# Kernel tuning notes

Hardware: AMD Instinct MI355X
Metric: run time of the kernel (lower is better)

The kernel has to match this reference:

```python
import jax, jax.numpy as jnp
import numpy as np

HEAD_DIM = 128
N_HEADS = 32
NEG_INF = -1e9


def apply_rope(x, cos, sin):
    # x: (B, S, H, D); cos/sin: (S, D//2). Pairs (x[...,2i], x[...,2i+1]) form
    # complex numbers (torch.view_as_complex on reshape(..., -1, 2)).
    xr = x[..., 0::2]
    xi = x[..., 1::2]
    c = cos[None, :, None, :]
    s = sin[None, :, None, :]
    out_r = xr * c - xi * s
    out_i = xr * s + xi * c
    return jnp.stack([out_r, out_i], axis=-1).reshape(x.shape)


def setup_inputs() -> dict:
    key = jax.random.key(0)
    ks = jax.random.split(key, 8)
    B, S, D = 2, 1024, 4096
    hd = HEAD_DIM
    x = jax.random.normal(ks[0], (B, S, D), dtype=jnp.float32)
    # true RoPE frequencies
    theta = 10000.0 ** (-np.arange(0, hd, 2, dtype=np.float32) / hd)  # (hd/2,)
    angles = np.arange(S, dtype=np.float32)[:, None] * theta[None, :]  # (S, hd/2)
    freqs_cos = jnp.asarray(np.cos(angles))
    freqs_sin = jnp.asarray(np.sin(angles))
    # causal additive mask
    mask = jnp.where(jnp.triu(jnp.ones((S, S), dtype=bool), k=1), NEG_INF, 0.0)
    mask = mask[None, None, :, :].astype(jnp.float32)
    scale = 0.02
    wq = jax.random.normal(ks[1], (D, D), dtype=jnp.float32) * scale
    wk = jax.random.normal(ks[2], (D, D), dtype=jnp.float32) * scale
    wv = jax.random.normal(ks[3], (D, D), dtype=jnp.float32) * scale
    wo = jax.random.normal(ks[4], (D, D), dtype=jnp.float32) * scale
    cache_k = jnp.zeros((B, S, N_HEADS, hd), dtype=jnp.float32)
    cache_v = jnp.zeros((B, S, N_HEADS, hd), dtype=jnp.float32)
    return {
        "x": x, "start_pos": 0, "freqs_cos": freqs_cos, "freqs_sin": freqs_sin,
        "mask": mask, "cache_k": cache_k, "cache_v": cache_v,
        "wq": wq, "wk": wk, "wv": wv, "wo": wo,
    }


def reference(x, start_pos, freqs_cos, freqs_sin, mask, cache_k, cache_v, wq, wk, wv, wo):
    B, S, D = x.shape
    H, hd = N_HEADS, HEAD_DIM
    # QKV projections (torch Linear: y = x @ W.T)
    xq = jnp.einsum('bsd,od->bso', x, wq).reshape(B, S, H, hd)
    xk = jnp.einsum('bsd,od->bso', x, wk).reshape(B, S, H, hd)
    xv = jnp.einsum('bsd,od->bso', x, wv).reshape(B, S, H, hd)
    xq = apply_rope(xq, freqs_cos, freqs_sin)
    xk = apply_rope(xk, freqs_cos, freqs_sin)
    # KV-cache append (n_rep == 1, so repeat_kv is identity)
    cache_k = jax.lax.dynamic_update_slice(cache_k, xk, (0, start_pos, 0, 0))
    cache_v = jax.lax.dynamic_update_slice(cache_v, xv, (0, start_pos, 0, 0))
    kv_len = start_pos + S
    keys = cache_k[:, :kv_len]
    values = cache_v[:, :kv_len]
    # attention: energy -> mask -> scaled softmax -> weighted sum
    energy = jnp.einsum('bqhd,bkhd->bhqk', xq, keys)
    energy = energy + mask
    scores = jax.nn.softmax(energy.astype(jnp.float32) / jnp.sqrt(jnp.float32(hd)), axis=-1).astype(xq.dtype)
    out = jnp.einsum('bhqk,bkhd->bqhd', scores, values).reshape(B, S, H * hd)
    return jnp.einsum('bso,do->bsd', out, wo)
```

## Files before the change

### kernel.cpp

```cpp
#include <hip/hip_runtime.h>
#include <hip/hip_bf16.h>
#include <stdint.h>
#include <stddef.h>

typedef __bf16 bf16_t;
typedef __attribute__((ext_vector_type(8))) __bf16 bf16x8;
typedef __attribute__((ext_vector_type(4))) float f32x4;
typedef __attribute__((ext_vector_type(16))) float f32x16;
typedef __attribute__((ext_vector_type(4))) uint32_t u32x4;

#define D_MODEL 4096
#define SEQ 1024
#define NH 32
#define HD 128
#define MTOT 2048

#define VMCNT(n) asm volatile("s_waitcnt vmcnt(" #n ")" ::: "memory")
#define LGKM0() asm volatile("s_waitcnt lgkmcnt(0)" ::: "memory")
#define SCHED0() __builtin_amdgcn_sched_barrier(0)

__device__ __forceinline__ void gload_lds16(const void* g, void* l) {
  __builtin_amdgcn_global_load_lds((const __attribute__((address_space(1))) uint32_t*)g,
                                   (__attribute__((address_space(3))) uint32_t*)l, 16, 0, 0);
}

__device__ __forceinline__ uint32_t cvtpk(float lo, float hi) {
  uint32_t r;
  asm("v_cvt_pk_bf16_f32 %0, %1, %2" : "=v"(r) : "v"(lo), "v"(hi));
  return r;
}
__device__ __forceinline__ void plswap(uint32_t& a, uint32_t& b) {
  asm volatile("v_permlane32_swap_b32 %0, %1" : "+v"(a), "+v"(b));
}

__global__ void dtype_probe(const uint32_t* __restrict__ x, uint32_t* __restrict__ flag) {
  const int lane = threadIdx.x & 63;
  const uint32_t w = x[lane];
  const uint32_t e = (w >> 7) & 0xFF;
  const bool inband = (e >= 100 && e <= 140);
  const unsigned long long m = __ballot(inband);
  if (lane == 0) *flag = (__popcll(m) >= 32) ? 1u : 0u;
}

__global__ __launch_bounds__(256) void conv_bf16(const void* __restrict__ src,
                                                 bf16_t* __restrict__ dst, int n,
                                                 const uint32_t* __restrict__ flag) {
  const int i = (blockIdx.x * 256 + threadIdx.x) * 8;
  if (i >= n) return;
  if (*flag) {
    *(bf16x8*)(dst + i) = *(const bf16x8*)((const bf16_t*)src + i);
  } else {
    const float4 a = *(const float4*)((const float*)src + i);
    const float4 b = *(const float4*)((const float*)src + i + 4);
    bf16x8 v;
    v[0] = (bf16_t)a.x; v[1] = (bf16_t)a.y; v[2] = (bf16_t)a.z; v[3] = (bf16_t)a.w;
    v[4] = (bf16_t)b.x; v[5] = (bf16_t)b.y; v[6] = (bf16_t)b.z; v[7] = (bf16_t)b.w;
    *(bf16x8*)(dst + i) = v;
  }
}

template <int MODE>
__global__ __launch_bounds__(512, 2) void gemm_bt(
    const bf16_t* __restrict__ A, const bf16_t* __restrict__ B,
    void* __restrict__ dstv, const uint32_t* __restrict__ flagp,
    const bf16_t* __restrict__ fcos, const bf16_t* __restrict__ fsin) {
  __shared__ __align__(16) char smem[3 * 49152];
  const int tid = threadIdx.x;
  const int lane = tid & 63, wid = tid >> 6;
  const int fr = lane & 15, fq = lane >> 4;
  const int wm = wid >> 2, wn = wid & 3;
  const int bm0 = blockIdx.x * 128, bn0 = blockIdx.y * 256;
  const bool isbf = (MODE == 2) ? (*flagp != 0) : true;

  auto stage_half = [&](int t, int bi, int h) {
    const int k0 = t * 64;
    char* ab = smem + bi * 49152;
    char* bb = ab + 16384;
    {
      const int o = h * 8192 + tid * 16;
      const int row = o >> 7, ch = (o >> 4) & 7;
      gload_lds16(A + (size_t)(bm0 + row) * D_MODEL + k0 + ((ch ^ (row & 7)) * 8), ab + o);
    }
#pragma unroll
    for (int j = 0; j < 2; ++j) {
      const int o = (h * 2 + j) * 8192 + tid * 16;
      const int row = o >> 7, ch = (o >> 4) & 7;
      gload_lds16(B + (size_t)(bn0 + row) * D_MODEL + k0 + ((ch ^ (row & 7)) * 8), bb + o);
    }
  };

  f32x4 acc[4][4];
#pragma unroll
  for (int m = 0; m < 4; m++)
#pragma unroll
    for (int n = 0; n < 4; n++) acc[m][n] = f32x4{0.f, 0.f, 0.f, 0.f};

  auto phase = [&](int bi, int kk, bool do_stage, int ts, int bs, int h) {
    const char* ab = smem + bi * 49152;
    const char* bb = ab + 16384;
    const int swz = ((kk * 4 + fq) ^ (fr & 7)) << 4;
    bf16x8 af[4], bfv[4];
#pragma unroll
    for (int m = 0; m < 4; ++m)
      af[m] = *(const bf16x8*)(ab + (wm * 64 + m * 16 + fr) * 128 + swz);
#pragma unroll
    for (int n = 0; n < 4; ++n)
      bfv[n] = *(const bf16x8*)(bb + (wn * 64 + n * 16 + fr) * 128 + swz);
    if (do_stage) stage_half(ts, bs, h);
    __builtin_amdgcn_s_barrier();
    LGKM0();
    SCHED0();
    __builtin_amdgcn_s_setprio(1);
#pragma unroll
    for (int m = 0; m < 4; ++m)
#pragma unroll
      for (int n = 0; n < 4; ++n)
        acc[m][n] = __builtin_amdgcn_mfma_f32_16x16x32_bf16(af[m], bfv[n], acc[m][n], 0, 0, 0);
    __builtin_amdgcn_s_setprio(0);
  };

  const int NT = D_MODEL / 64;
  stage_half(0, 0, 0); stage_half(0, 0, 1);
  stage_half(1, 1, 0); stage_half(1, 1, 1);
  VMCNT(6);
  __builtin_amdgcn_s_barrier();
  SCHED0();
  int cur = 0, nxt = 2;
  for (int t = 0; t < NT - 2; ++t) {
    phase(cur, 0, true, t + 2, nxt, 0);
    __builtin_amdgcn_s_barrier();
    phase(cur, 1, true, t + 2, nxt, 1);
    VMCNT(6);
    __builtin_amdgcn_s_barrier();
    SCHED0();
    cur = (cur == 2) ? 0 : cur + 1;
    nxt = (nxt == 2) ? 0 : nxt + 1;
  }
  phase(cur, 0, false, 0, 0, 0);
  __builtin_amdgcn_s_barrier();
  phase(cur, 1, false, 0, 0, 0);
  VMCNT(0);
  __builtin_amdgcn_s_barrier();
  SCHED0();
  cur = (cur == 2) ? 0 : cur + 1;
  phase(cur, 0, false, 0, 0, 0);
  __builtin_amdgcn_s_barrier();
  phase(cur, 1, false, 0, 0, 0);

#pragma unroll
  for (int m = 0; m < 4; m++) {
#pragma unroll
    for (int n = 0; n < 4; n++) {
      const int gn = bn0 + wn * 64 + n * 16 + fr;
#pragma unroll
      for (int r = 0; r < 4; r++) {
        const int gm = bm0 + wm * 64 + m * 16 + fq * 4 + r;
        const float vv = acc[m][n][r];
        if constexpr (MODE == 0) {
          const float pv = __shfl_xor(vv, 1);
          const int s = gm & (SEQ - 1);
          const int i = (gn & (HD - 1)) >> 1;
          const float c = (float)fcos[s * 64 + i];
          const float si = (float)fsin[s * 64 + i];
          const float outv = (gn & 1) ? (pv * si + vv * c) : (vv * c - pv * si);
          const int b = gm >> 10, h = gn >> 7, dd = gn & (HD - 1);
          ((bf16_t*)dstv)[((size_t)(b * NH + h) * SEQ + s) * HD + dd] = (bf16_t)outv;
        } else if constexpr (MODE == 1) {
          const int b = gm >> 10, s = gm & (SEQ - 1), h = gn >> 7, dd = gn & (HD - 1);
          ((bf16_t*)dstv)[((size_t)(b * NH + h) * HD + dd) * SEQ + s] = (bf16_t)vv;
        } else {
          if (isbf) ((bf16_t*)dstv)[(size_t)gm * D_MODEL + gn] = (bf16_t)vv;
          else      ((float*)dstv)[(size_t)gm * D_MODEL + gn] = vv;
        }
      }
    }
  }
}

__global__ __launch_bounds__(512, 2) void attn_fwd(
    const bf16_t* __restrict__ Q, const bf16_t* __restrict__ K,
    const bf16_t* __restrict__ V, bf16_t* __restrict__ Out) {
  constexpr float SC = 0.088388347648318447f;
  constexpr float MNEG = -10000.0f;
  __shared__ __align__(16) char smem[65536];
  const int tid = threadIdx.x, lane = tid & 63, wid = tid >> 6;
  const int l31 = lane & 31, hi = lane >> 5, l7 = lane & 7;
  const int qt = 3 - (int)blockIdx.x;
  const int bh = blockIdx.y;
  const int qb0 = qt * 256;
  const int q0w = qb0 + wid * 32;
  const int nt = qt * 4 + 4;

  const bf16_t* Kbase = K + (size_t)bh * SEQ * HD;
  const bf16_t* Vbase = V + (size_t)bh * HD * SEQ;

  bf16x8 qa[8];
  {
    const bf16_t* qp = Q + ((size_t)bh * SEQ + q0w + l31) * HD + hi * 8;
#pragma unroll
    for (int ks = 0; ks < 8; ++ks) qa[ks] = *(const bf16x8*)(qp + ks * 16);
  }

  auto stage = [&](int t, int bi) {
    const int kv0 = t * 64;
#pragma unroll
    for (int pass = 0; pass < 2; ++pass) {
      const int o = pass * 8192 + tid * 16;
      {
        const int row = o >> 8, ch = (o & 255) >> 4;
        gload_lds16(Kbase + (size_t)(kv0 + row) * HD + ((ch ^ (row & 7)) * 8),
                    smem + bi * 16384 + o);
      }
      {
        const int row = o >> 7, ch = (o & 127) >> 4;
        gload_lds16(Vbase + (size_t)row * SEQ + kv0 + ((ch ^ (row & 7)) * 8),
                    smem + 32768 + bi * 16384 + o);
      }
    }
  };

  f32x16 Oacc[4];
#pragma unroll
  for (int i = 0; i < 4; ++i)
#pragma unroll
    for (int j = 0; j < 16; ++j) Oacc[i][j] = 0.f;
  float mrow = MNEG, lrow = 0.f;

  stage(0, 0);
  stage(1, 1);
  VMCNT(4);
  __builtin_amdgcn_s_barrier();

  for (int t = 0; t < nt; ++t) {
    const int kv0 = t * 64;
    if (kv0 < q0w + 32) {
      const char* kb_ = smem + (t & 1) * 16384;
      const char* vb_ = smem + 32768 + (t & 1) * 16384;

      f32x16 sacc[2];
#pragma unroll
      for (int kb = 0; kb < 2; ++kb)
#pragma unroll
        for (int j = 0; j < 16; ++j) sacc[kb][j] = 0.f;
      __builtin_amdgcn_s_setprio(1);
#pragma unroll
      for (int kb = 0; kb < 2; ++kb)
#pragma unroll
        for (int ks = 0; ks < 8; ++ks) {
          bf16x8 kf = *(const bf16x8*)(kb_ + (kb * 32 + l31) * 256 +
                                       (((ks * 2 + hi) ^ l7) << 4));
          sacc[kb] = __builtin_amdgcn_mfma_f32_32x32x16_bf16(kf, qa[ks], sacc[kb], 0, 0, 0);
        }
      __builtin_amdgcn_s_setprio(0);

      const bool diag = (kv0 + 63 > q0w);
      float pm = MNEG;
#pragma unroll
      for (int kb = 0; kb < 2; ++kb)
#pragma unroll
        for (int r = 0; r < 16; ++r) {
          float x = sacc[kb][r] * SC;
          if (diag) {
            const int kvpos = kv0 + kb * 32 + (r & 3) + 8 * (r >> 2) + 4 * hi;
            if (kvpos > q0w + l31) x = MNEG;
          }
          sacc[kb][r] = x;
          pm = fmaxf(pm, x);
        }
      pm = fmaxf(pm, __shfl_xor(pm, 32));
      const float mn = fmaxf(mrow, pm);
      const float al = __expf(mrow - mn);
      mrow = mn;
      float ps = 0.f;
#pragma unroll
      for (int kb = 0; kb < 2; ++kb)
#pragma unroll
        for (int r = 0; r < 16; ++r) {
          const float e = __expf(sacc[kb][r] - mn);
          sacc[kb][r] = e;
          ps += e;
        }
      lrow = lrow * al + ps;
#pragma unroll
      for (int db = 0; db < 4; ++db)
#pragma unroll
        for (int j = 0; j < 16; ++j) Oacc[db][j] *= al;

      uint32_t pw[16];
#pragma unroll
      for (int kb = 0; kb < 2; ++kb) {
        const int o8 = kb * 8;
        pw[o8 + 0] = cvtpk(sacc[kb][0], sacc[kb][1]);
        pw[o8 + 1] = cvtpk(sacc[kb][2], sacc[kb][3]);
        pw[o8 + 2] = cvtpk(sacc[kb][4], sacc[kb][5]);
        pw[o8 + 3] = cvtpk(sacc[kb][6], sacc[kb][7]);
        plswap(pw[o8 + 0], pw[o8 + 2]);
        plswap(pw[o8 + 1], pw[o8 + 3]);
        pw[o8 + 4] = cvtpk(sacc[kb][8], sacc[kb][9]);
        pw[o8 + 5] = cvtpk(sacc[kb][10], sacc[kb][11]);
        pw[o8 + 6] = cvtpk(sacc[kb][12], sacc[kb][13]);
        pw[o8 + 7] = cvtpk(sacc[kb][14], sacc[kb][15]);
        plswap(pw[o8 + 4], pw[o8 + 6]);
        plswap(pw[o8 + 5], pw[o8 + 7]);
      }

      __builtin_amdgcn_s_setprio(1);
#pragma unroll
      for (int db = 0; db < 4; ++db)
#pragma unroll
        for (int ks2 = 0; ks2 < 4; ++ks2) {
          bf16x8 vf = *(const bf16x8*)(vb_ + (db * 32 + l31) * 128 +
                                       (((ks2 * 2 + hi) ^ l7) << 4));
          union { u32x4 u; bf16x8 v; } pc;
          pc.u = u32x4{pw[ks2 * 4], pw[ks2 * 4 + 1], pw[ks2 * 4 + 2], pw[ks2 * 4 + 3]};
          Oacc[db] = __builtin_amdgcn_mfma_f32_32x32x16_bf16(vf, pc.v, Oacc[db], 0, 0, 0);
        }
      __builtin_amdgcn_s_setprio(0);
    }

    __builtin_amdgcn_s_barrier();
    if (t + 2 < nt) {
      stage(t + 2, t & 1);
      VMCNT(4);
    } else if (t + 1 < nt) {
      VMCNT(0);
    }
    __builtin_amdgcn_s_barrier();
  }

  lrow += __shfl_xor(lrow, 32);
  const float linv = 1.0f / fmaxf(lrow, 1e-20f);

  {
    char* ob = smem + wid * 8192;
#pragma unroll
    for (int db = 0; db < 4; ++db)
#pragma unroll
      for (int rp = 0; rp < 8; ++rp) {
        const int r = rp * 2;
        const int d = db * 32 + (r & 3) + 8 * (r >> 2) + 4 * hi;
        const uint32_t w = cvtpk(Oacc[db][r] * linv, Oacc[db][r + 1] * linv);
        *(uint32_t*)(ob + l31 * 256 + ((d * 2) ^ ((l31 & 7) << 4))) = w;
      }
  }
  __builtin_amdgcn_s_barrier();
  const int b = bh >> 5, h = bh & 31;
#pragma unroll
  for (int pass = 0; pass < 8; ++pass) {
    const int o = pass * 8192 + tid * 16;
    const int row = o >> 8, ch = (o & 255) >> 4;
    const u32x4 val = *(const u32x4*)(smem + row * 256 + ((ch ^ (row & 7)) << 4));
    *(u32x4*)(Out + ((size_t)(b * SEQ + qb0 + row)) * D_MODEL + h * HD + ch * 8) = val;
  }
}

extern "C" void kernel_launch(void* const* d_in, const int* in_sizes, int n_in,
                              void* d_out, int out_size, void* d_ws, size_t ws_size,
                              hipStream_t stream) {
  (void)in_sizes; (void)n_in; (void)out_size;
  const void* x_raw    = d_in[0];
  const void* fcos_raw = d_in[2];
  const void* fsin_raw = d_in[3];
  const void* wq_raw   = d_in[7];
  const void* wk_raw   = d_in[8];
  const void* wv_raw   = d_in[9];
  const void* wo_raw   = d_in[10];

  const size_t NX = (size_t)MTOT * D_MODEL;
  const size_t NW = (size_t)D_MODEL * D_MODEL;
  const size_t NF = SEQ * (HD / 2);

  char* base = (char*)d_ws;
  uint32_t* flag = (uint32_t*)base;
  bf16_t* fc = (bf16_t*)(base + 4096);
  bf16_t* fs = (bf16_t*)(base + 4096 + 131072);
  bf16_t* elems = (bf16_t*)(base + (1 << 20));
  bf16_t* xc = elems;
  bf16_t* w0 = xc + NX;
  bf16_t* w1 = w0 + NW;
  bf16_t* q_ws = w1 + NW;
  bf16_t* k_ws = q_ws + NX;
  bf16_t* v_ws = k_ws + NX;
  bf16_t* a_ws = v_ws + NX;
  const size_t NEED = (1 << 20) + 2 * (5 * NX + 2 * NW);
  if (ws_size < NEED) return;

  dtype_probe<<<1, 64, 0, stream>>>((const uint32_t*)x_raw, flag);

  const int cb_x = (int)(NX / (256 * 8));
  const int cb_w = (int)(NW / (256 * 8));
  const int cb_f = (int)(NF / (256 * 8));
  conv_bf16<<<cb_x, 256, 0, stream>>>(x_raw, xc, (int)NX, flag);
  conv_bf16<<<cb_f, 256, 0, stream>>>(fcos_raw, fc, (int)NF, flag);
  conv_bf16<<<cb_f, 256, 0, stream>>>(fsin_raw, fs, (int)NF, flag);

  dim3 gg(MTOT / 128, D_MODEL / 256);
  conv_bf16<<<cb_w, 256, 0, stream>>>(wq_raw, w0, (int)NW, flag);
  gemm_bt<0><<<gg, 512, 0, stream>>>(xc, w0, q_ws, flag, fc, fs);
  conv_bf16<<<cb_w, 256, 0, stream>>>(wk_raw, w1, (int)NW, flag);
  gemm_bt<0><<<gg, 512, 0, stream>>>(xc, w1, k_ws, flag, fc, fs);
  conv_bf16<<<cb_w, 256, 0, stream>>>(wv_raw, w0, (int)NW, flag);
  gemm_bt<1><<<gg, 512, 0, stream>>>(xc, w0, v_ws, flag, fc, fs);

  attn_fwd<<<dim3(4, 2 * NH), 512, 0, stream>>>(q_ws, k_ws, v_ws, a_ws);

  conv_bf16<<<cb_w, 256, 0, stream>>>(wo_raw, w1, (int)NW, flag);
  gemm_bt<2><<<gg, 512, 0, stream>>>(a_ws, w1, d_out, flag, fc, fs);
}
```

Before: 400.0 us.

## Fuse fp32-to-bf16 weight conversion into GEMM B-operand loading

Removes the four separate weight conversion kernels and their bf16 workspace buffers. The GEMM now loads raw fp32 weight tiles into registers, converts them to bf16, and writes them swizzled into LDS, double-buffered across iterations. This saves a full read and write of each 64MB weight matrix but changes the B path from async direct-to-LDS loads to register staging, which raises register pressure and may weaken overlap. Each GEMM block also rereads fp32 B, so it fetches twice the bytes per tile compared with bf16.

Measured after the change: 1.592 ms. 298% more time.

```diff
diff --git a/kernel.cpp b/kernel.cpp
--- a/kernel.cpp
+++ b/kernel.cpp
@@ -61,7 +61,7 @@
 
 template <int MODE>
 __global__ __launch_bounds__(512, 2) void gemm_bt(
-    const bf16_t* __restrict__ A, const bf16_t* __restrict__ B,
+    const bf16_t* __restrict__ A, const void* __restrict__ Braw,
     void* __restrict__ dstv, const uint32_t* __restrict__ flagp,
     const bf16_t* __restrict__ fcos, const bf16_t* __restrict__ fsin) {
   __shared__ __align__(16) char smem[3 * 49152];
@@ -70,24 +70,57 @@
   const int fr = lane & 15, fq = lane >> 4;
   const int wm = wid >> 2, wn = wid & 3;
   const int bm0 = blockIdx.x * 128, bn0 = blockIdx.y * 256;
-  const bool isbf = (MODE == 2) ? (*flagp != 0) : true;
-
-  auto stage_half = [&](int t, int bi, int h) {
+  const bool isbf = (*flagp != 0);
+  const int brow = tid >> 1, bhalf = tid & 1;
+
+  auto stageA = [&](int t, int bi) {
     const int k0 = t * 64;
     char* ab = smem + bi * 49152;
-    char* bb = ab + 16384;
-    {
-      const int o = h * 8192 + tid * 16;
+#pragma unroll
+    for (int p = 0; p < 2; ++p) {
+      const int o = p * 8192 + tid * 16;
       const int row = o >> 7, ch = (o >> 4) & 7;
       gload_lds16(A + (size_t)(bm0 + row) * D_MODEL + k0 + ((ch ^ (row & 7)) * 8), ab + o);
     }
-#pragma unroll
-    for (int j = 0; j < 2; ++j) {
-      const int o = (h * 2 + j) * 8192 + tid * 16;
-      const int row = o >> 7, ch = (o >> 4) & 7;
-      gload_lds16(B + (size_t)(bn0 + row) * D_MODEL + k0 + ((ch ^ (row & 7)) * 8), bb + o);
-    }
   };
+  auto issueB = [&](float4 (&st)[8], int t) {
+    const int k0 = t * 64;
+    if (isbf) {
+      const bf16_t* bp = (const bf16_t*)Braw + (size_t)(bn0 + brow) * D_MODEL + k0 + bhalf * 32;
+#pragma unroll
+      for (int j = 0; j < 8; ++j) {
+        const uint2 v = *(const uint2*)(bp + j * 4);
+        st[j].x = __uint_as_float(v.x);
+        st[j].y = __uint_as_float(v.y);
+      }
+    } else {
+      const float* bp = (const float*)Braw + (size_t)(bn0 + brow) * D_MODEL + k0 + bhalf * 32;
+#pragma unroll
+      for (int j = 0; j < 8; ++j) st[j] = *(const float4*)(bp + j * 4);
+    }
+  };
+  auto writeB = [&](float4 (&st)[8], int bi) {
+    char* bb = smem + bi * 49152 + 16384;
+    uint32_t pw[16];
+    if (isbf) {
+#pragma unroll
+      for (int j = 0; j < 8; ++j) {
+        pw[2 * j] = __float_as_uint(st[j].x);
+        pw[2 * j + 1] = __float_as_uint(st[j].y);
+      }
+    } else {
+#pragma unroll
+      for (int j = 0; j < 8; ++j) {
+        pw[2 * j] = cvtpk(st[j].x, st[j].y);
+        pw[2 * j + 1] = cvtpk(st[j].z, st[j].w);
+      }
+    }
+#pragma unroll
+    for (int c = 0; c < 4; ++c) {
+      const u32x4 v{pw[4 * c], pw[4 * c + 1], pw[4 * c + 2], pw[4 * c + 3]};
+      *(u32x4*)(bb + brow * 128 + (((bhalf * 4 + c) ^ (brow & 7)) << 4)) = v;
+    }
+  };
 
   f32x4 acc[4][4];
 #pragma unroll
@@ -95,7 +128,7 @@
 #pragma unroll
     for (int n = 0; n < 4; n++) acc[m][n] = f32x4{0.f, 0.f, 0.f, 0.f};
 
-  auto phase = [&](int bi, int kk, bool do_stage, int ts, int bs, int h) {
+  auto phase = [&](int bi, int kk, bool doA, int tA, int biA) {
     const char* ab = smem + bi * 49152;
     const char* bb = ab + 16384;
     const int swz = ((kk * 4 + fq) ^ (fr & 7)) << 4;
@@ -106,7 +139,7 @@
 #pragma unroll
     for (int n = 0; n < 4; ++n)
       bfv[n] = *(const bf16x8*)(bb + (wn * 64 + n * 16 + fr) * 128 + swz);
-    if (do_stage) stage_half(ts, bs, h);
+    if (doA) stageA(tA, biA);
     __builtin_amdgcn_s_barrier();
     LGKM0();
     SCHED0();
@@ -120,32 +153,53 @@
   };
 
   const int NT = D_MODEL / 64;
-  stage_half(0, 0, 0); stage_half(0, 0, 1);
-  stage_half(1, 1, 0); stage_half(1, 1, 1);
-  VMCNT(6);
-  __builtin_amdgcn_s_barrier();
-  SCHED0();
+  float4 rA[8], rB[8];
+  stageA(0, 0);
+  issueB(rA, 0);
+  VMCNT(0);
+  writeB(rA, 0);
+  stageA(1, 1);
+  issueB(rA, 1);
+  LGKM0();
+  __builtin_amdgcn_s_barrier();
   int cur = 0, nxt = 2;
-  for (int t = 0; t < NT - 2; ++t) {
-    phase(cur, 0, true, t + 2, nxt, 0);
-    __builtin_amdgcn_s_barrier();
-    phase(cur, 1, true, t + 2, nxt, 1);
-    VMCNT(6);
-    __builtin_amdgcn_s_barrier();
-    SCHED0();
-    cur = (cur == 2) ? 0 : cur + 1;
-    nxt = (nxt == 2) ? 0 : nxt + 1;
-  }
-  phase(cur, 0, false, 0, 0, 0);
-  __builtin_amdgcn_s_barrier();
-  phase(cur, 1, false, 0, 0, 0);
+  for (int tt = 0; tt < NT - 2; tt += 2) {
+    {
+      phase(cur, 0, true, tt + 2, nxt);
+      __builtin_amdgcn_s_barrier();
+      phase(cur, 1, false, 0, 0);
+      VMCNT(2);
+      issueB(rB, tt + 2);
+      writeB(rA, (cur == 2) ? 0 : cur + 1);
+      LGKM0();
+      __builtin_amdgcn_s_barrier();
+      cur = (cur == 2) ? 0 : cur + 1;
+      nxt = (nxt == 2) ? 0 : nxt + 1;
+    }
+    {
+      phase(cur, 0, true, tt + 3, nxt);
+      __builtin_amdgcn_s_barrier();
+      phase(cur, 1, false, 0, 0);
+      VMCNT(2);
+      issueB(rA, tt + 3);
+      writeB(rB, (cur == 2) ? 0 : cur + 1);
+      LGKM0();
+      __builtin_amdgcn_s_barrier();
+      cur = (cur == 2) ? 0 : cur + 1;
+      nxt = (nxt == 2) ? 0 : nxt + 1;
+    }
+  }
+  phase(cur, 0, false, 0, 0);
+  __builtin_amdgcn_s_barrier();
+  phase(cur, 1, false, 0, 0);
   VMCNT(0);
-  __builtin_amdgcn_s_barrier();
-  SCHED0();
+  writeB(rA, (cur == 2) ? 0 : cur + 1);
+  LGKM0();
+  __builtin_amdgcn_s_barrier();
   cur = (cur == 2) ? 0 : cur + 1;
-  phase(cur, 0, false, 0, 0, 0);
-  __builtin_amdgcn_s_barrier();
-  phase(cur, 1, false, 0, 0, 0);
+  phase(cur, 0, false, 0, 0);
+  __builtin_amdgcn_s_barrier();
+  phase(cur, 1, false, 0, 0);
 
 #pragma unroll
   for (int m = 0; m < 4; m++) {
@@ -376,34 +430,27 @@
   bf16_t* fs = (bf16_t*)(base + 4096 + 131072);
   bf16_t* elems = (bf16_t*)(base + (1 << 20));
   bf16_t* xc = elems;
-  bf16_t* w0 = xc + NX;
-  bf16_t* w1 = w0 + NW;
-  bf16_t* q_ws = w1 + NW;
+  bf16_t* q_ws = xc + NX;
   bf16_t* k_ws = q_ws + NX;
   bf16_t* v_ws = k_ws + NX;
   bf16_t* a_ws = v_ws + NX;
-  const size_t NEED = (1 << 20) + 2 * (5 * NX + 2 * NW);
+  const size_t NEED = (1 << 20) + 2 * (5 * NX);
   if (ws_size < NEED) return;
 
   dtype_probe<<<1, 64, 0, stream>>>((const uint32_t*)x_raw, flag);
 
   const int cb_x = (int)(NX / (256 * 8));
-  const int cb_w = (int)(NW / (256 * 8));
   const int cb_f = (int)(NF / (256 * 8));
   conv_bf16<<<cb_x, 256, 0, stream>>>(x_raw, xc, (int)NX, flag);
   conv_bf16<<<cb_f, 256, 0, stream>>>(fcos_raw, fc, (int)NF, flag);
   conv_bf16<<<cb_f, 256, 0, stream>>>(fsin_raw, fs, (int)NF, flag);
 
   dim3 gg(MTOT / 128, D_MODEL / 256);
-  conv_bf16<<<cb_w, 256, 0, stream>>>(wq_raw, w0, (int)NW, flag);
-  gemm_bt<0><<<gg, 512, 0, stream>>>(xc, w0, q_ws, flag, fc, fs);
-  conv_bf16<<<cb_w, 256, 0, stream>>>(wk_raw, w1, (int)NW, flag);
-  gemm_bt<0><<<gg, 512, 0, stream>>>(xc, w1, k_ws, flag, fc, fs);
-  conv_bf16<<<cb_w, 256, 0, stream>>>(wv_raw, w0, (int)NW, flag);
-  gemm_bt<1><<<gg, 512, 0, stream>>>(xc, w0, v_ws, flag, fc, fs);
+  gemm_bt<0><<<gg, 512, 0, stream>>>(xc, wq_raw, q_ws, flag, fc, fs);
+  gemm_bt<0><<<gg, 512, 0, stream>>>(xc, wk_raw, k_ws, flag, fc, fs);
+  gemm_bt<1><<<gg, 512, 0, stream>>>(xc, wv_raw, v_ws, flag, fc, fs);
 
   attn_fwd<<<dim3(4, 2 * NH), 512, 0, stream>>>(q_ws, k_ws, v_ws, a_ws);
 
-  conv_bf16<<<cb_w, 256, 0, stream>>>(wo_raw, w1, (int)NW, flag);
-  gemm_bt<2><<<gg, 512, 0, stream>>>(a_ws, w1, d_out, flag, fc, fs);
-}
+  gemm_bt<2><<<gg, 512, 0, stream>>>(a_ws, wo_raw, d_out, flag, fc, fs);
+}
```
